# Performance work log

Hardware: AMD Instinct MI355X
Metric: run time of the kernel (lower is better)

The kernel has to match this reference:

```python
import jax, jax.numpy as jnp
import numpy as np

NUM_HEADS = 16
HEAD_DIM = 64
HIDDEN = NUM_HEADS * HEAD_DIM


def _rotate_half(x):
    half = x.shape[-1] // 2
    x1, x2 = x[..., :half], x[..., half:]
    return jnp.concatenate([-x2, x1], axis=-1)


def setup_inputs() -> dict:
    key = jax.random.key(0)
    k1, k2, k3, k4, k5 = jax.random.split(key, 5)
    B, T = 2, 2048
    x = jax.random.normal(k1, (B, T, HIDDEN), dtype=jnp.float32)
    # rotary tables (seq_len, head_dim) as in apply_rope docstring
    cos = jax.random.uniform(k2, (T, HEAD_DIM), dtype=jnp.float32)
    sin = jax.random.uniform(k3, (T, HEAD_DIM), dtype=jnp.float32)
    # nn.Linear weights: y = x @ W.T ; scaled for stable fp32 activations
    w_qkv = jax.random.normal(k4, (3 * HIDDEN, HIDDEN), dtype=jnp.float32) * (1.0 / np.sqrt(HIDDEN))
    w_out = jax.random.normal(k5, (HIDDEN, HIDDEN), dtype=jnp.float32) * (1.0 / np.sqrt(HIDDEN))
    return {"x": x, "cos": cos, "sin": sin, "w_qkv": w_qkv, "w_out": w_out}


def reference(x, cos, sin, w_qkv, w_out):
    B, T, C = x.shape
    H, D = NUM_HEADS, HEAD_DIM
    qkv = jnp.einsum("btc,fc->btf", x, w_qkv)          # (B, T, 3C)
    q, k, v = jnp.split(qkv, 3, axis=-1)
    # (B, T, C) -> (B, H, T, D)
    to_heads = lambda t: t.reshape(B, T, H, D).transpose(0, 2, 1, 3)
    q, k, v = to_heads(q), to_heads(k), to_heads(v)
    # RoPE: broadcast cos/sin (T, D) over batch and heads
    cos_b = cos[None, None, :, :]
    sin_b = sin[None, None, :, :]
    q = q * cos_b + _rotate_half(q) * sin_b
    k = k * cos_b + _rotate_half(k) * sin_b
    # causal scaled dot-product attention (dropout_p = 0 in eval)
    scale = 1.0 / np.sqrt(D)
    scores = jnp.einsum("bhqd,bhkd->bhqk", q, k) * scale  # (B, H, T, T)
    causal = jnp.tril(jnp.ones((T, T), dtype=bool))
    scores = jnp.where(causal[None, None], scores, jnp.finfo(scores.dtype).min)
    probs = jax.nn.softmax(scores, axis=-1)
    out = jnp.einsum("bhqk,bhkd->bhqd", probs, v)          # (B, H, T, D)
    out = out.transpose(0, 2, 1, 3).reshape(B, T, C)
    return jnp.einsum("btc,fc->btf", out, w_out)
```

## Files before the change

### kernel.cpp

```cpp
#include <hip/hip_runtime.h>

typedef unsigned short u16;
typedef __bf16 bf16x8 __attribute__((ext_vector_type(8)));
typedef __bf16 bf16x4 __attribute__((ext_vector_type(4)));
typedef float f32x4 __attribute__((ext_vector_type(4)));

__device__ __forceinline__ u16 f2bf(float f) {
    union { float f; unsigned int i; } v; v.f = f;
    unsigned int x = v.i;
    x += 0x7fffu + ((x >> 16) & 1u);
    return (u16)(x >> 16);
}

__device__ __forceinline__ void gl_lds16(const u16* g, u16* l) {
    __builtin_amdgcn_global_load_lds(
        (const __attribute__((address_space(1))) void*)g,
        (__attribute__((address_space(3))) void*)l, 16, 0, 0);
}

__global__ __launch_bounds__(256, 2)
void cvt_xw_kernel(const float* __restrict__ X, const float* __restrict__ Wq,
                   u16* __restrict__ Xb, u16* __restrict__ Wqb)
{
    const int n1 = 4194304 / 4;
    const int n2 = 3145728 / 4;
    int i = blockIdx.x * 256 + threadIdx.x;
    const int stride = gridDim.x * 256;
    for (; i < n1 + n2; i += stride) {
        float4 v;
        ushort4* dst;
        if (i < n1) { v = ((const float4*)X)[i];       dst = (ushort4*)Xb + i; }
        else        { v = ((const float4*)Wq)[i - n1]; dst = (ushort4*)Wqb + (i - n1); }
        ushort4 o;
        o.x = f2bf(v.x); o.y = f2bf(v.y); o.z = f2bf(v.z); o.w = f2bf(v.w);
        *dst = o;
    }
}

__global__ __launch_bounds__(256, 2)
void cvt_w_kernel(const float* __restrict__ W, u16* __restrict__ Wb)
{
    int i = blockIdx.x * 256 + threadIdx.x;
    float4 v = ((const float4*)W)[i];
    ushort4 o;
    o.x = f2bf(v.x); o.y = f2bf(v.y); o.z = f2bf(v.z); o.w = f2bf(v.w);
    ((ushort4*)Wb)[i] = o;
}

__global__ __launch_bounds__(256, 2)
void qkv_rope_kernel(const u16* __restrict__ X, const u16* __restrict__ W,
                     const float* __restrict__ Cos, const float* __restrict__ Sin,
                     u16* __restrict__ Qo, u16* __restrict__ Ko, u16* __restrict__ Vo)
{
    __shared__ __align__(16) u16 As[128 * 64];
    __shared__ __align__(16) u16 Bs[128 * 64];
    const int tid  = threadIdx.x;
    const int lane = tid & 63, wave = tid >> 6;
    const int l15  = lane & 15, q4 = lane >> 4;
    const int wm = (wave >> 1) * 64, wn = (wave & 1) * 64;
    const int m0 = blockIdx.y * 128, n0 = blockIdx.x * 128;
    const int srow = lane >> 3;
    const int scol = ((lane & 7) ^ srow) * 8;

    f32x4 acc[4][4];
    #pragma unroll
    for (int i = 0; i < 4; i++)
        #pragma unroll
        for (int j = 0; j < 4; j++) { f32x4 z = {}; acc[i][j] = z; }

    for (int k0 = 0; k0 < 1024; k0 += 64) {
        __syncthreads();
        #pragma unroll
        for (int i = 0; i < 4; i++) {
            int rb = wave * 32 + i * 8;
            gl_lds16(X + (size_t)(m0 + rb + srow) * 1024 + k0 + scol, As + rb * 64);
            gl_lds16(W + (size_t)(n0 + rb + srow) * 1024 + k0 + scol, Bs + rb * 64);
        }
        __syncthreads();
        #pragma unroll
        for (int ks = 0; ks < 2; ks++) {
            const int ch = (((4 * ks + q4) ^ (l15 & 7)) * 8);
            bf16x8 af[4], bfr[4];
            #pragma unroll
            for (int i = 0; i < 4; i++) {
                af[i]  = *(const bf16x8*)&As[(wm + i * 16 + l15) * 64 + ch];
                bfr[i] = *(const bf16x8*)&Bs[(wn + i * 16 + l15) * 64 + ch];
            }
            #pragma unroll
            for (int mi = 0; mi < 4; mi++)
                #pragma unroll
                for (int ni = 0; ni < 4; ni++)
                    acc[mi][ni] = __builtin_amdgcn_mfma_f32_16x16x32_bf16(
                        af[mi], bfr[ni], acc[mi][ni], 0, 0, 0);
        }
    }

    #pragma unroll
    for (int mi = 0; mi < 4; mi++) {
        #pragma unroll
        for (int r = 0; r < 4; r++) {
            int row = m0 + wm + mi * 16 + q4 * 4 + r;
            int b = row >> 11, t = row & 2047;
            #pragma unroll
            for (int ni = 0; ni < 4; ni++) {
                int col = n0 + wn + ni * 16 + l15;
                float v = acc[mi][ni][r];
                int sec = col >> 10;
                int hh  = (col >> 6) & 15;
                int d   = col & 63;
                if (sec < 2) {
                    float cs = Cos[t * 64 + d];
                    float sn = Sin[t * 64 + d];
                    float partner = acc[mi][ni ^ 2][r];
                    float rot = (d < 32) ? -partner : partner;
                    v = v * cs + rot * sn;
                    u16* dst = (sec == 0) ? Qo : Ko;
                    dst[(((size_t)(b * 16 + hh)) * 2048 + t) * 64 + d] = f2bf(v);
                } else {
                    Vo[(((size_t)(b * 16 + hh)) * 64 + d) * 2048 + t] = f2bf(v);
                }
            }
        }
    }
}

__global__ __launch_bounds__(256, 3)
void attn_kernel(const u16* __restrict__ Q, const u16* __restrict__ Kg,
                 const u16* __restrict__ Vt, u16* __restrict__ Oh)
{
    __shared__ __align__(16) u16 Ks[128 * 64];
    __shared__ __align__(16) u16 Vs[64 * 128];
    __shared__ __align__(16) __bf16 Ps[4][16][136];

    const int bx = blockIdx.x;
    const int xcd = bx & 7;
    const int i8  = bx >> 3;
    const int bh  = xcd * 4 + (i8 & 3);
    const int qt  = 31 - (i8 >> 2);
    const int b = bh >> 4, h = bh & 15;
    const int tid = threadIdx.x, wave = tid >> 6, lane = tid & 63;
    const int l15 = lane & 15, q4 = lane >> 4;
    const int srow = lane >> 3;
    const int sKcol = ((lane & 7) ^ srow) * 8;

    const size_t head_off = (size_t)bh * 2048 * 64;
    const u16* Qb = Q  + head_off;
    const u16* Kb = Kg + head_off;
    const u16* Vb = Vt + head_off;

    const int qrow0 = qt * 64 + wave * 16;

    bf16x8 qf[2];
    #pragma unroll
    for (int ks = 0; ks < 2; ks++) {
        bf16x8 t = *(const bf16x8*)(Qb + (size_t)(qrow0 + l15) * 64 + ks * 32 + q4 * 8);
        #pragma unroll
        for (int j = 0; j < 8; j++) t[j] = (__bf16)((float)t[j] * 0.125f);
        qf[ks] = t;
    }

    bf16x8 ones;
    #pragma unroll
    for (int j = 0; j < 8; j++) ones[j] = (__bf16)1.0f;

    f32x4 o[4];
    f32x4 ol = {};
    float mstq = -1e30f;
    #pragma unroll
    for (int ni = 0; ni < 4; ni++) { f32x4 z = {}; o[ni] = z; }

    const int nkv = (qt >> 1) + 1;
    for (int it = 0; it < nkv; it++) {
        const int k0 = it * 128;
        __syncthreads();
        #pragma unroll
        for (int i = 0; i < 8; i++) {
            int id = wave * 8 + i;
            if (id < 16) {
                int rb = id * 8;
                gl_lds16(Kb + (size_t)(k0 + rb + srow) * 64 + sKcol, Ks + rb * 64);
            } else {
                int rb = (id - 16) * 4;
                int d  = rb + (lane >> 4);
                int cl = ((lane & 15) ^ (d & 15)) * 8;
                gl_lds16(Vb + (size_t)d * 2048 + k0 + cl, Vs + rb * 128);
            }
        }
        __syncthreads();

        f32x4 st[2][4];
        #pragma unroll
        for (int hf = 0; hf < 2; hf++)
            #pragma unroll
            for (int mi = 0; mi < 4; mi++) { f32x4 z = {}; st[hf][mi] = z; }
        #pragma unroll
        for (int ks = 0; ks < 2; ks++) {
            const int ch = (((4 * ks + q4) ^ (l15 & 7)) * 8);
            #pragma unroll
            for (int hf = 0; hf < 2; hf++) {
                bf16x8 kf[4];
                #pragma unroll
                for (int mi = 0; mi < 4; mi++)
                    kf[mi] = *(const bf16x8*)&Ks[(hf * 64 + mi * 16 + l15) * 64 + ch];
                #pragma unroll
                for (int mi = 0; mi < 4; mi++)
                    st[hf][mi] = __builtin_amdgcn_mfma_f32_16x16x32_bf16(
                        kf[mi], qf[ks], st[hf][mi], 0, 0, 0);
            }
        }

        float rm = -1e30f;
        if (it == nkv - 1) {
            const int tq = qrow0 + l15;
            #pragma unroll
            for (int hf = 0; hf < 2; hf++)
                #pragma unroll
                for (int mi = 0; mi < 4; mi++)
                    #pragma unroll
                    for (int r = 0; r < 4; r++) {
                        float v = st[hf][mi][r];
                        if (k0 + hf * 64 + mi * 16 + q4 * 4 + r > tq) v = -1e30f;
                        st[hf][mi][r] = v;
                        rm = fmaxf(rm, v);
                    }
        } else {
            #pragma unroll
            for (int hf = 0; hf < 2; hf++)
                #pragma unroll
                for (int mi = 0; mi < 4; mi++)
                    #pragma unroll
                    for (int r = 0; r < 4; r++)
                        rm = fmaxf(rm, st[hf][mi][r]);
        }
        rm = fmaxf(rm, __shfl_xor(rm, 16, 64));
        rm = fmaxf(rm, __shfl_xor(rm, 32, 64));

        float mnew  = fmaxf(mstq, rm);
        float alpha = __expf(mstq - mnew);
        mstq = mnew;

        #pragma unroll
        for (int hf = 0; hf < 2; hf++)
            #pragma unroll
            for (int mi = 0; mi < 4; mi++) {
                bf16x4 p4;
                #pragma unroll
                for (int r = 0; r < 4; r++)
                    p4[r] = (__bf16)__expf(st[hf][mi][r] - mnew);
                *(bf16x4*)&Ps[wave][l15][hf * 64 + mi * 16 + q4 * 4] = p4;
            }

        float ar[4];
        #pragma unroll
        for (int r = 0; r < 4; r++)
            ar[r] = __shfl(alpha, q4 * 4 + r, 64);
        #pragma unroll
        for (int ni = 0; ni < 4; ni++)
            #pragma unroll
            for (int r = 0; r < 4; r++)
                o[ni][r] *= ar[r];
        #pragma unroll
        for (int r = 0; r < 4; r++)
            ol[r] *= ar[r];

        #pragma unroll
        for (int ks = 0; ks < 4; ks++) {
            bf16x8 pa = *(const bf16x8*)&Ps[wave][l15][ks * 32 + q4 * 8];
            bf16x8 vf[4];
            #pragma unroll
            for (int ni = 0; ni < 4; ni++) {
                const int pc = (((ks * 4 + q4) ^ l15) * 8);
                vf[ni] = *(const bf16x8*)&Vs[(ni * 16 + l15) * 128 + pc];
            }
            #pragma unroll
            for (int ni = 0; ni < 4; ni++)
                o[ni] = __builtin_amdgcn_mfma_f32_16x16x32_bf16(pa, vf[ni], o[ni], 0, 0, 0);
            ol = __builtin_amdgcn_mfma_f32_16x16x32_bf16(pa, ones, ol, 0, 0, 0);
        }
    }

    #pragma unroll
    for (int r = 0; r < 4; r++) {
        int t = qrow0 + q4 * 4 + r;
        float inv = 1.0f / ol[r];
        #pragma unroll
        for (int ni = 0; ni < 4; ni++) {
            int d = ni * 16 + l15;
            Oh[(((size_t)(b * 2048 + t)) * 16 + h) * 64 + d] = f2bf(o[ni][r] * inv);
        }
    }
}

__global__ __launch_bounds__(256, 2)
void outproj_kernel(const u16* __restrict__ A, const u16* __restrict__ W,
                    float* __restrict__ Cout)
{
    __shared__ __align__(16) u16 As[128 * 64];
    __shared__ __align__(16) u16 Bs[64 * 64];
    const int tid  = threadIdx.x;
    const int lane = tid & 63, wave = tid >> 6;
    const int l15  = lane & 15, q4 = lane >> 4;
    const int wm = (wave >> 1) * 64, wn = (wave & 1) * 32;
    const int m0 = blockIdx.y * 128, n0 = blockIdx.x * 64;
    const int srow = lane >> 3;
    const int scol = ((lane & 7) ^ srow) * 8;

    f32x4 acc[4][2];
    #pragma unroll
    for (int i = 0; i < 4; i++)
        #pragma unroll
        for (int j = 0; j < 2; j++) { f32x4 z = {}; acc[i][j] = z; }

    for (int k0 = 0; k0 < 1024; k0 += 64) {
        __syncthreads();
        #pragma unroll
        for (int i = 0; i < 6; i++) {
            int id = wave * 6 + i;
            if (id < 16) {
                int rb = id * 8;
                gl_lds16(A + (size_t)(m0 + rb + srow) * 1024 + k0 + scol, As + rb * 64);
            } else {
                int rb = (id - 16) * 8;
                gl_lds16(W + (size_t)(n0 + rb + srow) * 1024 + k0 + scol, Bs + rb * 64);
            }
        }
        __syncthreads();
        #pragma unroll
        for (int ks = 0; ks < 2; ks++) {
            const int ch = (((4 * ks + q4) ^ (l15 & 7)) * 8);
            bf16x8 af[4], bfr[2];
            #pragma unroll
            for (int i = 0; i < 4; i++)
                af[i] = *(const bf16x8*)&As[(wm + i * 16 + l15) * 64 + ch];
            #pragma unroll
            for (int ni = 0; ni < 2; ni++)
                bfr[ni] = *(const bf16x8*)&Bs[(wn + ni * 16 + l15) * 64 + ch];
            #pragma unroll
            for (int mi = 0; mi < 4; mi++)
                #pragma unroll
                for (int ni = 0; ni < 2; ni++)
                    acc[mi][ni] = __builtin_amdgcn_mfma_f32_16x16x32_bf16(
                        af[mi], bfr[ni], acc[mi][ni], 0, 0, 0);
        }
    }

    #pragma unroll
    for (int mi = 0; mi < 4; mi++)
        #pragma unroll
        for (int r = 0; r < 4; r++) {
            int row = m0 + wm + mi * 16 + q4 * 4 + r;
            #pragma unroll
            for (int ni = 0; ni < 2; ni++) {
                int col = n0 + wn + ni * 16 + l15;
                Cout[(size_t)row * 1024 + col] = acc[mi][ni][r];
            }
        }
}

extern "C" void kernel_launch(void* const* d_in, const int* in_sizes, int n_in,
                              void* d_out, int out_size, void* d_ws, size_t ws_size,
                              hipStream_t stream) {
    (void)in_sizes; (void)n_in; (void)out_size; (void)ws_size;
    const float* x     = (const float*)d_in[0];
    const float* cosp  = (const float*)d_in[1];
    const float* sinp  = (const float*)d_in[2];
    const float* w_qkv = (const float*)d_in[3];
    const float* w_out = (const float*)d_in[4];
    float* out = (float*)d_out;

    const size_t NELEM = (size_t)2 * 2048 * 1024;
    u16* Q   = (u16*)d_out;
    u16* Xb  = (u16*)d_out + NELEM;
    u16* K   = (u16*)d_ws;
    u16* Vt  = K + NELEM;
    u16* Oh  = Vt + NELEM;
    u16* Wqb = Oh;
    u16* Wob = K;

    cvt_xw_kernel<<<7168, 256, 0, stream>>>(x, w_qkv, Xb, Wqb);
    qkv_rope_kernel<<<dim3(24, 32), 256, 0, stream>>>(Xb, Wqb, cosp, sinp, Q, K, Vt);
    attn_kernel<<<1024, 256, 0, stream>>>(Q, K, Vt, Oh);
    cvt_w_kernel<<<1024, 256, 0, stream>>>(w_out, Wob);
    outproj_kernel<<<dim3(16, 32), 256, 0, stream>>>(Oh, Wob, out);
}
```

Baseline: 190.4 us.

## Vectorize V-transpose stores and retile out-projection GEMM to 64x64x128

```diff
diff --git a/kernel.cpp b/kernel.cpp
--- a/kernel.cpp
+++ b/kernel.cpp
@@ -95,20 +95,36 @@
         }
     }
 
-    #pragma unroll
-    for (int mi = 0; mi < 4; mi++) {
-        #pragma unroll
-        for (int r = 0; r < 4; r++) {
-            int row = m0 + wm + mi * 16 + q4 * 4 + r;
-            int b = row >> 11, t = row & 2047;
+    if (n0 >= 2048) {
+        #pragma unroll
+        for (int mi = 0; mi < 4; mi++) {
+            int t0row = m0 + wm + mi * 16 + q4 * 4;
+            int b = t0row >> 11, t0 = t0row & 2047;
             #pragma unroll
             for (int ni = 0; ni < 4; ni++) {
                 int col = n0 + wn + ni * 16 + l15;
-                float v = acc[mi][ni][r];
-                int sec = col >> 10;
                 int hh  = (col >> 6) & 15;
                 int d   = col & 63;
-                if (sec < 2) {
+                ushort4 pk;
+                pk.x = f2bf(acc[mi][ni][0]); pk.y = f2bf(acc[mi][ni][1]);
+                pk.z = f2bf(acc[mi][ni][2]); pk.w = f2bf(acc[mi][ni][3]);
+                *(ushort4*)&Vo[(((size_t)(b * 16 + hh)) * 64 + d) * 2048 + t0] = pk;
+            }
+        }
+    } else {
+        #pragma unroll
+        for (int mi = 0; mi < 4; mi++) {
+            #pragma unroll
+            for (int r = 0; r < 4; r++) {
+                int row = m0 + wm + mi * 16 + q4 * 4 + r;
+                int b = row >> 11, t = row & 2047;
+                #pragma unroll
+                for (int ni = 0; ni < 4; ni++) {
+                    int col = n0 + wn + ni * 16 + l15;
+                    float v = acc[mi][ni][r];
+                    int sec = col >> 10;
+                    int hh  = (col >> 6) & 15;
+                    int d   = col & 63;
                     float cs = Cos[t * 64 + d];
                     float sn = Sin[t * 64 + d];
                     float partner = acc[mi][ni ^ 2][r];
@@ -116,8 +132,6 @@
                     v = v * cs + rot * sn;
                     u16* dst = (sec == 0) ? Qo : Ko;
                     dst[(((size_t)(b * 16 + hh)) * 2048 + t) * 64 + d] = f2bf(v);
-                } else {
-                    Vo[(((size_t)(b * 16 + hh)) * 64 + d) * 2048 + t] = f2bf(v);
                 }
             }
         }
@@ -291,52 +305,49 @@
     }
 }
 
-__global__ __launch_bounds__(256, 2)
+__global__ __launch_bounds__(256, 4)
 void outproj_kernel(const u16* __restrict__ A, const u16* __restrict__ W,
                     float* __restrict__ Cout)
 {
-    __shared__ __align__(16) u16 As[128 * 64];
-    __shared__ __align__(16) u16 Bs[64 * 64];
+    __shared__ __align__(16) u16 As[64 * 128];
+    __shared__ __align__(16) u16 Bs[64 * 128];
     const int tid  = threadIdx.x;
     const int lane = tid & 63, wave = tid >> 6;
     const int l15  = lane & 15, q4 = lane >> 4;
-    const int wm = (wave >> 1) * 64, wn = (wave & 1) * 32;
-    const int m0 = blockIdx.y * 128, n0 = blockIdx.x * 64;
-    const int srow = lane >> 3;
-    const int scol = ((lane & 7) ^ srow) * 8;
-
-    f32x4 acc[4][2];
-    #pragma unroll
-    for (int i = 0; i < 4; i++)
+    const int wm = (wave >> 1) * 32, wn = (wave & 1) * 32;
+    const int m0 = blockIdx.y * 64, n0 = blockIdx.x * 64;
+
+    f32x4 acc[2][2];
+    #pragma unroll
+    for (int i = 0; i < 2; i++)
         #pragma unroll
         for (int j = 0; j < 2; j++) { f32x4 z = {}; acc[i][j] = z; }
 
-    for (int k0 = 0; k0 < 1024; k0 += 64) {
-        __syncthreads();
-        #pragma unroll
-        for (int i = 0; i < 6; i++) {
-            int id = wave * 6 + i;
-            if (id < 16) {
-                int rb = id * 8;
-                gl_lds16(A + (size_t)(m0 + rb + srow) * 1024 + k0 + scol, As + rb * 64);
-            } else {
-                int rb = (id - 16) * 8;
-                gl_lds16(W + (size_t)(n0 + rb + srow) * 1024 + k0 + scol, Bs + rb * 64);
-            }
-        }
-        __syncthreads();
-        #pragma unroll
-        for (int ks = 0; ks < 2; ks++) {
-            const int ch = (((4 * ks + q4) ^ (l15 & 7)) * 8);
-            bf16x8 af[4], bfr[2];
-            #pragma unroll
-            for (int i = 0; i < 4; i++)
-                af[i] = *(const bf16x8*)&As[(wm + i * 16 + l15) * 64 + ch];
-            #pragma unroll
-            for (int ni = 0; ni < 2; ni++)
-                bfr[ni] = *(const bf16x8*)&Bs[(wn + ni * 16 + l15) * 64 + ch];
-            #pragma unroll
-            for (int mi = 0; mi < 4; mi++)
+    for (int k0 = 0; k0 < 1024; k0 += 128) {
+        __syncthreads();
+        #pragma unroll
+        for (int i = 0; i < 8; i++) {
+            int id = wave * 8 + i;
+            int rb = (id & 15) * 4;
+            int row = rb + (lane >> 4);
+            int cl  = ((lane & 15) ^ (row & 15)) * 8;
+            if (id < 16)
+                gl_lds16(A + (size_t)(m0 + row) * 1024 + k0 + cl, As + rb * 128);
+            else
+                gl_lds16(W + (size_t)(n0 + row) * 1024 + k0 + cl, Bs + rb * 128);
+        }
+        __syncthreads();
+        #pragma unroll
+        for (int ks = 0; ks < 4; ks++) {
+            const int ch = (((ks * 4 + q4) ^ l15) * 8);
+            bf16x8 af[2], bfr[2];
+            #pragma unroll
+            for (int i = 0; i < 2; i++) {
+                af[i]  = *(const bf16x8*)&As[(wm + i * 16 + l15) * 128 + ch];
+                bfr[i] = *(const bf16x8*)&Bs[(wn + i * 16 + l15) * 128 + ch];
+            }
+            #pragma unroll
+            for (int mi = 0; mi < 2; mi++)
                 #pragma unroll
                 for (int ni = 0; ni < 2; ni++)
                     acc[mi][ni] = __builtin_amdgcn_mfma_f32_16x16x32_bf16(
@@ -345,7 +356,7 @@
     }
 
     #pragma unroll
-    for (int mi = 0; mi < 4; mi++)
+    for (int mi = 0; mi < 2; mi++)
         #pragma unroll
         for (int r = 0; r < 4; r++) {
             int row = m0 + wm + mi * 16 + q4 * 4 + r;
@@ -381,5 +392,5 @@
     qkv_rope_kernel<<<dim3(24, 32), 256, 0, stream>>>(Xb, Wqb, cosp, sinp, Q, K, Vt);
     attn_kernel<<<1024, 256, 0, stream>>>(Q, K, Vt, Oh);
     cvt_w_kernel<<<1024, 256, 0, stream>>>(w_out, Wob);
-    outproj_kernel<<<dim3(16, 32), 256, 0, stream>>>(Oh, Wob, out);
-}
+    outproj_kernel<<<dim3(16, 64), 256, 0, stream>>>(Oh, Wob, out);
+}
```

New measurement: 178.3 us. 1.07x faster.
